# Kernel optimization log

Measured on AMD Instinct MI355X. Metric: run time of the kernel, lower is better.

## Reference

```python
import jax, jax.numpy as jnp
import numpy as np

B, I, D = 8192, 1000, 1000   # batch of candidates, rated items, item feature dim
E, ATT, D1, D2 = 64, 16, 64, 32  # embed size, attention hidden, MLP dense1/dense2


def setup_inputs() -> dict:
    key = jax.random.key(0)
    ks = jax.random.split(key, 16)
    init = lambda k, shape, fan_in: (jax.random.normal(k, shape, jnp.float32) / np.sqrt(fan_in))
    return {
        "candidate_items": jax.random.normal(ks[0], (B, D), jnp.float32),
        "rated_items": jax.random.normal(ks[1], (I, D), jnp.float32),
        "user_matrix": jax.random.uniform(ks[2], (B, I), jnp.float32),
        # item_embeddings: Linear(D, E)
        "We": init(ks[3], (E, D), D), "be": jnp.zeros((E,), jnp.float32),
        # AttentionNet: Linear(2E, ATT) -> ReLU -> Linear(ATT, 1)
        "Wa1": init(ks[4], (ATT, 2 * E), 2 * E), "ba1": jnp.zeros((ATT,), jnp.float32),
        "Wa2": init(ks[5], (1, ATT), ATT), "ba2": jnp.zeros((1,), jnp.float32),
        # MLP: Linear(2E, D1) -> ReLU -> Linear(D1, D2) -> ReLU -> Linear(D2, 1)
        "Wm1": init(ks[6], (D1, 2 * E), 2 * E), "bm1": jnp.zeros((D1,), jnp.float32),
        "Wm2": init(ks[7], (D2, D1), D1), "bm2": jnp.zeros((D2,), jnp.float32),
        "Wm3": init(ks[8], (1, D2), D2), "bm3": jnp.zeros((1,), jnp.float32),
    }


def reference(candidate_items, rated_items, user_matrix,
              We, be, Wa1, ba1, Wa2, ba2, Wm1, bm1, Wm2, bm2, Wm3, bm3):
    # item embeddings
    e_c = candidate_items @ We.T + be                    # [B, E]
    # rated embeddings are .detach()'d in the original
    e_r = jax.lax.stop_gradient(rated_items @ We.T + be) # [I, E]
    e_c_sg = jax.lax.stop_gradient(e_c)                  # detached for attention

    # Additive attention over concat([cand, rated]): split Wa1 into cand/rated halves
    # so the per-i loop becomes one broadcasted op producing [B, I, ATT].
    W1c, W1r = Wa1[:, :E], Wa1[:, E:]
    h = jax.nn.relu(e_c_sg @ W1c.T[:, None, :].reshape(1, 1, -1).reshape(E, ATT)[None][0] if False else
                    (e_c_sg @ W1c.T)[:, None, :] + (e_r @ W1r.T)[None, :, :] + ba1)  # [B, I, ATT]
    scores = jnp.einsum('bia,a->bi', h, Wa2[0]) + ba2[0]  # [B, I]
    att = jax.nn.softmax(scores, axis=1)                  # [B, I]

    # attention-weighted user profile -> user embedding
    user_emb = (att * user_matrix) @ e_r                  # [B, E]

    # MLP head (dropout inactive: eval mode)
    x = jnp.concatenate([e_c, user_emb], axis=1)          # [B, 2E]
    x = jax.nn.relu(x @ Wm1.T + bm1)
    x = jax.nn.relu(x @ Wm2.T + bm2)
    return x @ Wm3.T + bm3                                # [B, 1]
```

## Files before the change

### kernel.cpp

```cpp
#include <hip/hip_runtime.h>

typedef unsigned short u16;
typedef unsigned int   u32;
typedef float f32x4  __attribute__((ext_vector_type(4)));
typedef short bf16x8 __attribute__((ext_vector_type(8)));
typedef short s16x4  __attribute__((ext_vector_type(4)));

__device__ __forceinline__ u16 f2b_rne(float x) {
    u32 u = __float_as_uint(x);
    return (u16)((u + 0x7fffu + ((u >> 16) & 1u)) >> 16);
}
__device__ __forceinline__ float b2f(u16 u) { return __uint_as_float((u32)u << 16); }
__device__ __forceinline__ void split1(float x, u16& h, u16& l) {
    h = f2b_rne(x);
    l = f2b_rne(x - b2f(h));
}
__device__ __forceinline__ void mk_frag(f32x4 a, f32x4 b, bf16x8& hi, bf16x8& lo) {
#pragma unroll
    for (int j = 0; j < 4; ++j) { u16 h, l; split1(a[j], h, l); hi[j] = (short)h; lo[j] = (short)l; }
#pragma unroll
    for (int j = 0; j < 4; ++j) { u16 h, l; split1(b[j], h, l); hi[4+j] = (short)h; lo[4+j] = (short)l; }
}

__global__ __launch_bounds__(1024, 8) void kemb_all(
    const float* __restrict__ cand, const float* __restrict__ rated,
    const float* __restrict__ We, const float* __restrict__ be,
    const float* __restrict__ Wa1, const float* __restrict__ Wm1,
    float* __restrict__ ec, u16* __restrict__ er_th, float* __restrict__ ar,
    u16* __restrict__ Wm1b)
{
    const int blk = blockIdx.x;
    if (blk == 63) {
        for (int idx = threadIdx.x; idx < 8192; idx += 1024)
            Wm1b[idx] = f2b_rne(Wm1[idx]);
        return;
    }
    const bool is_rated = (blk < 64);
    const int  i0    = is_rated ? blk * 16 : (blk - 64) * 16;
    const int  Mrows = is_rated ? 1000 : 8192;
    const float* X   = is_rated ? rated : cand;

    __shared__ u16 S16[2 * 16 * 1008];
    float* Sf = (float*)S16;
    u16* XH = S16;
    u16* XL = S16 + 16 * 1008;

    const int t    = threadIdx.x;
    const int wv   = t >> 6;
    const int lane = t & 63;

    {
        const int r    = wv;
        const int arow = min(i0 + r, Mrows - 1);
        const float* xr = X + (size_t)arow * 1000;
#pragma unroll
        for (int j = 0; j < 4; ++j) {
            const int k4 = lane + j * 64;
            if (k4 < 250) {
                f32x4 v = *(const f32x4*)(xr + k4 * 4);
                s16x4 h4, l4;
#pragma unroll
                for (int jj = 0; jj < 4; ++jj) {
                    u16 hh, ll; split1(v[jj], hh, ll);
                    h4[jj] = (short)hh; l4[jj] = (short)ll;
                }
                *(s16x4*)(XH + r * 1008 + k4 * 4) = h4;
                *(s16x4*)(XL + r * 1008 + k4 * 4) = l4;
            }
        }
    }
    __syncthreads();

    const int l15 = lane & 15, q = lane >> 4;
    const int ct = wv & 3, h = wv >> 2;
    f32x4 acc = {0.f, 0.f, 0.f, 0.f};
    {
        const u16* ahp = XH + l15 * 1008;
        const u16* alp = XL + l15 * 1008;
        const float* wr = We + (size_t)(ct * 16 + l15) * 1000;

        const int kc0 = h * 256;
        const int kc1 = (h == 3) ? 992 : kc0 + 256;
        for (int kc = kc0; kc < kc1; kc += 32) {
            bf16x8 ah = *(const bf16x8*)(ahp + kc + q * 8);
            bf16x8 al = *(const bf16x8*)(alp + kc + q * 8);
            bf16x8 bh, bl;
            mk_frag(*(const f32x4*)(wr + kc + q * 8), *(const f32x4*)(wr + kc + q * 8 + 4), bh, bl);
            acc = __builtin_amdgcn_mfma_f32_16x16x32_bf16(ah, bh, acc, 0, 0, 0);
            acc = __builtin_amdgcn_mfma_f32_16x16x32_bf16(ah, bl, acc, 0, 0, 0);
            acc = __builtin_amdgcn_mfma_f32_16x16x32_bf16(al, bh, acc, 0, 0, 0);
        }
        if (h == 3) {
            bf16x8 ah = {0,0,0,0,0,0,0,0}, al = {0,0,0,0,0,0,0,0};
            bf16x8 bh = {0,0,0,0,0,0,0,0}, bl = {0,0,0,0,0,0,0,0};
            if (q == 0) {
                ah = *(const bf16x8*)(ahp + 992);
                al = *(const bf16x8*)(alp + 992);
                mk_frag(*(const f32x4*)(wr + 992), *(const f32x4*)(wr + 996), bh, bl);
            }
            acc = __builtin_amdgcn_mfma_f32_16x16x32_bf16(ah, bh, acc, 0, 0, 0);
            acc = __builtin_amdgcn_mfma_f32_16x16x32_bf16(ah, bl, acc, 0, 0, 0);
            acc = __builtin_amdgcn_mfma_f32_16x16x32_bf16(al, bh, acc, 0, 0, 0);
        }
    }
    __syncthreads();
#pragma unroll
    for (int r = 0; r < 4; ++r)
        Sf[h * 1024 + (q * 4 + r) * 64 + ct * 16 + l15] = acc[r];
    __syncthreads();

    {
        const int b = t >> 6, e = t & 63;
        float v = be[e] + Sf[b * 64 + e] + Sf[1024 + b * 64 + e]
                        + Sf[2048 + b * 64 + e] + Sf[3072 + b * 64 + e];
        if (!is_rated) {
            ec[(size_t)(i0 + b) * 64 + e] = v;
        } else {
            if (i0 + b < 1000) er_th[(size_t)e * 1000 + (i0 + b)] = f2b_rne(v);
            Sf[4096 + b * 68 + e] = v;
        }
    }

    if (is_rated) {
        __syncthreads();
        if (wv == 0) {
            f32x4 a2 = {0.f, 0.f, 0.f, 0.f};
#pragma unroll
            for (int kc = 0; kc < 64; kc += 32) {
                const float* ap = Sf + 4096 + l15 * 68 + kc + q * 8;
                const float* bp = Wa1 + l15 * 128 + 64 + kc + q * 8;
                bf16x8 ah, al, bh, bl;
                mk_frag(*(const f32x4*)ap, *(const f32x4*)(ap + 4), ah, al);
                mk_frag(*(const f32x4*)bp, *(const f32x4*)(bp + 4), bh, bl);
                a2 = __builtin_amdgcn_mfma_f32_16x16x32_bf16(ah, bh, a2, 0, 0, 0);
                a2 = __builtin_amdgcn_mfma_f32_16x16x32_bf16(ah, bl, a2, 0, 0, 0);
                a2 = __builtin_amdgcn_mfma_f32_16x16x32_bf16(al, bh, a2, 0, 0, 0);
            }
#pragma unroll
            for (int r = 0; r < 4; ++r) {
                int i = i0 + q * 4 + r;
                if (i < 1000) ar[(size_t)i * 16 + l15] = a2[r];
            }
        }
    }
}

__global__ __launch_bounds__(1024, 8) void k3v10(
    const float* __restrict__ ar, const float* __restrict__ ecC,
    const u16* __restrict__ er_th, const float* __restrict__ um,
    const float* __restrict__ Wa1, const float* __restrict__ ba1,
    const float* __restrict__ Wa2, const u16* __restrict__ Wm1b,
    const float* __restrict__ bm1,
    const float* __restrict__ Wm2, const float* __restrict__ bm2,
    const float* __restrict__ Wm3, const float* __restrict__ bm3,
    float* __restrict__ out)
{
    __shared__ u16   S16[16 * 1032];
    __shared__ float ACL[256];
    __shared__ float SUMS[16];
    __shared__ u16   XB16[16 * 136];
    float* Sf = (float*)S16;
    const int t  = threadIdx.x;
    const int b0 = blockIdx.x * 16;

    if (t < 256) {
        const int a = t & 15, b = t >> 4;
        float acc = ba1[a];
        const float* ecr = ecC + (size_t)(b0 + b) * 64;
        const float* w = Wa1 + a * 128;
#pragma unroll 8
        for (int e = 0; e < 64; ++e) acc += ecr[e] * w[e];
        ACL[b * 16 + a] = acc;
    }
    __syncthreads();

    {
        const int i = t;
        if (i < 1000) {
            const f32x4* a4 = (const f32x4*)(ar + (size_t)i * 16);
            f32x4 r0 = a4[0], r1 = a4[1], r2 = a4[2], r3 = a4[3];
            float w2[16];
#pragma unroll
            for (int a = 0; a < 16; ++a) w2[a] = Wa2[a];
#pragma unroll 4
            for (int b = 0; b < 16; ++b) {
                const f32x4* ac4 = (const f32x4*)(ACL + b * 16);
                f32x4 c0 = ac4[0], c1 = ac4[1], c2 = ac4[2], c3 = ac4[3];
                float s0 = 0.f, s1 = 0.f;
                s0 += fmaxf(c0[0] + r0[0], 0.f) * w2[0];
                s1 += fmaxf(c0[1] + r0[1], 0.f) * w2[1];
                s0 += fmaxf(c0[2] + r0[2], 0.f) * w2[2];
                s1 += fmaxf(c0[3] + r0[3], 0.f) * w2[3];
                s0 += fmaxf(c1[0] + r1[0], 0.f) * w2[4];
                s1 += fmaxf(c1[1] + r1[1], 0.f) * w2[5];
                s0 += fmaxf(c1[2] + r1[2], 0.f) * w2[6];
                s1 += fmaxf(c1[3] + r1[3], 0.f) * w2[7];
                s0 += fmaxf(c2[0] + r2[0], 0.f) * w2[8];
                s1 += fmaxf(c2[1] + r2[1], 0.f) * w2[9];
                s0 += fmaxf(c2[2] + r2[2], 0.f) * w2[10];
                s1 += fmaxf(c2[3] + r2[3], 0.f) * w2[11];
                s0 += fmaxf(c3[0] + r3[0], 0.f) * w2[12];
                s1 += fmaxf(c3[1] + r3[1], 0.f) * w2[13];
                s0 += fmaxf(c3[2] + r3[2], 0.f) * w2[14];
                s1 += fmaxf(c3[3] + r3[3], 0.f) * w2[15];
                S16[b * 1032 + i] = f2b_rne(s0 + s1);
            }
        }
    }
    __syncthreads();

    {
        const int b = t >> 6, g = t & 63;
        float sv[16], uv[16];
#pragma unroll
        for (int k = 0; k < 16; ++k) {
            int i = g + 64 * k;
            sv[k] = (i < 1000) ? b2f(S16[b * 1032 + i]) : -1e30f;
        }
        float m = -1e30f;
#pragma unroll
        for (int k = 0; k < 16; ++k) m = fmaxf(m, sv[k]);
#pragma unroll
        for (int k = 1; k < 64; k <<= 1) m = fmaxf(m, __shfl_xor(m, k));
        const float* umr = um + (size_t)(b0 + b) * 1000;
#pragma unroll
        for (int k = 0; k < 16; ++k) {
            int i = g + 64 * k;
            uv[k] = (i < 1000) ? umr[i] : 0.f;
        }
        float sum = 0.f;
#pragma unroll
        for (int k = 0; k < 16; ++k) {
            int i = g + 64 * k;
            if (i < 1000) {
                float w = __expf(sv[k] - m);
                sum += w;
                S16[b * 1032 + i] = f2b_rne(w * uv[k]);
            }
        }
#pragma unroll
        for (int k = 1; k < 64; k <<= 1) sum += __shfl_xor(sum, k);
        if (g == 0) SUMS[b] = 1.0f / sum;
    }
    __syncthreads();

    {
        const int wv = t >> 6, lane = t & 63, l15 = lane & 15, q = lane >> 4;
        const int et = wv & 3, h = wv >> 2;
        const u16* php = S16 + l15 * 1032;
        const u16* bhp = er_th + (size_t)(et * 16 + l15) * 1000;
        f32x4 acc = {0.f, 0.f, 0.f, 0.f};

        const int kc0 = h * 256;
        const int kc1 = (h == 3) ? 992 : kc0 + 256;
        for (int kc = kc0; kc < kc1; kc += 32) {
            bf16x8 ah = *(const bf16x8*)(php + kc + q * 8);
            bf16x8 bh = *(const bf16x8*)(bhp + kc + q * 8);
            acc = __builtin_amdgcn_mfma_f32_16x16x32_bf16(ah, bh, acc, 0, 0, 0);
        }
        if (h == 3) {
            bf16x8 ah = {0,0,0,0,0,0,0,0}, bh = {0,0,0,0,0,0,0,0};
            if (q == 0) {
                ah = *(const bf16x8*)(php + 992);
                bh = *(const bf16x8*)(bhp + 992);
            }
            acc = __builtin_amdgcn_mfma_f32_16x16x32_bf16(ah, bh, acc, 0, 0, 0);
        }
        __syncthreads();
#pragma unroll
        for (int r = 0; r < 4; ++r)
            Sf[h * 1024 + (q * 4 + r) * 64 + et * 16 + l15] = acc[r];
    }
    __syncthreads();

    {
        const int b = t >> 6, e = t & 63;
        float v = (Sf[b * 64 + e] + Sf[1024 + b * 64 + e]
                 + Sf[2048 + b * 64 + e] + Sf[3072 + b * 64 + e]) * SUMS[b];
        XB16[b * 136 + 64 + e] = f2b_rne(v);
        XB16[b * 136 + e] = f2b_rne(ecC[(size_t)(b0 + b) * 64 + e]);
    }
    __syncthreads();

    {
        const int wv = t >> 6, lane = t & 63, l15 = lane & 15, q = lane >> 4;
        const int nt = wv & 3, kh = wv >> 2;
        bf16x8 ah = *(const bf16x8*)(XB16 + l15 * 136 + kh * 32 + q * 8);
        bf16x8 bh = *(const bf16x8*)(Wm1b + (size_t)(nt * 16 + l15) * 128 + kh * 32 + q * 8);
        f32x4 acc = {0.f, 0.f, 0.f, 0.f};
        acc = __builtin_amdgcn_mfma_f32_16x16x32_bf16(ah, bh, acc, 0, 0, 0);
#pragma unroll
        for (int r = 0; r < 4; ++r)
            Sf[kh * 1024 + (q * 4 + r) * 64 + nt * 16 + l15] = acc[r];
    }
    __syncthreads();

    {
        const int b = t >> 6, o = t & 63;
        float a = bm1[o] + Sf[b * 64 + o] + Sf[1024 + b * 64 + o]
                + Sf[2048 + b * 64 + o] + Sf[3072 + b * 64 + o];
        Sf[4096 + b * 64 + o] = fmaxf(a, 0.f);
    }
    __syncthreads();

    {
        const int b = t >> 6, j = t & 63;
        if (j < 32) {
            float a = bm2[j];
            const float* wr = Wm2 + j * 64;
            const float* x = Sf + 4096 + b * 64;
#pragma unroll 8
            for (int k = 0; k < 64; ++k) a += x[k] * wr[k];
            Sf[5120 + b * 32 + j] = fmaxf(a, 0.f);
        }
    }
    __syncthreads();

    {
        const int b = t >> 6, j = t & 63;
        float p = (j < 32) ? Sf[5120 + b * 32 + j] * Wm3[j] : 0.f;
#pragma unroll
        for (int kk = 1; kk < 64; kk <<= 1) p += __shfl_xor(p, kk);
        if (j == 0) out[b0 + b] = p + bm3[0];
    }
}

extern "C" void kernel_launch(void* const* d_in, const int* in_sizes, int n_in,
                              void* d_out, int out_size, void* d_ws, size_t ws_size,
                              hipStream_t stream) {
    const float* cand  = (const float*)d_in[0];
    const float* rated = (const float*)d_in[1];
    const float* um    = (const float*)d_in[2];
    const float* We    = (const float*)d_in[3];
    const float* be    = (const float*)d_in[4];
    const float* Wa1   = (const float*)d_in[5];
    const float* ba1   = (const float*)d_in[6];
    const float* Wa2   = (const float*)d_in[7];
    const float* Wm1   = (const float*)d_in[9];
    const float* bm1   = (const float*)d_in[10];
    const float* Wm2   = (const float*)d_in[11];
    const float* bm2   = (const float*)d_in[12];
    const float* Wm3   = (const float*)d_in[13];
    const float* bm3   = (const float*)d_in[14];

    float* arw   = (float*)d_ws;
    float* ec    = arw + 16000;
    u16*   er_th = (u16*)(ec + 524288);
    u16*   wm1b  = er_th + 64000;
    float* out   = (float*)d_out;

    kemb_all<<<dim3(576), dim3(1024), 0, stream>>>(cand, rated, We, be, Wa1, Wm1,
                                                   ec, er_th, arw, wm1b);
    k3v10   <<<dim3(512), dim3(1024), 0, stream>>>(arw, ec, er_th, um,
                                                   Wa1, ba1, Wa2, wm1b, bm1,
                                                   Wm2, bm2, Wm3, bm3, out);
}
```

Measured before the change: 163.5 us.

## Fuse embedding and attention kernels into one cooperative kernel with grid sync

Merges the embedding GEMM kernel and the attention/MLP kernel into a single cooperative launch. Each block computes its own candidate embeddings into shared memory, so they no longer round-trip through global memory. Every eighth block also computes a tile of the rated-item embeddings before a grid-wide sync. This removes one launch boundary and the global writes and reads of the candidate embeddings. In exchange it adds a grid barrier, it makes a few blocks do extra work before the barrier (load imbalance), and it requires all 512 blocks of 1024 threads to be co-resident. If the cooperative launch fails, the code falls back to a two-kernel path. A user_matrix load is also moved earlier to overlap with the max-reduction.

```diff
diff --git a/kernel.cpp b/kernel.cpp
--- a/kernel.cpp
+++ b/kernel.cpp
@@ -1,4 +1,7 @@
 #include <hip/hip_runtime.h>
+#include <hip/hip_cooperative_groups.h>
+
+namespace cg = cooperative_groups;
 
 typedef unsigned short u16;
 typedef unsigned int   u32;
@@ -22,36 +25,13 @@
     for (int j = 0; j < 4; ++j) { u16 h, l; split1(b[j], h, l); hi[4+j] = (short)h; lo[4+j] = (short)l; }
 }
 
-__global__ __launch_bounds__(1024, 8) void kemb_all(
-    const float* __restrict__ cand, const float* __restrict__ rated,
-    const float* __restrict__ We, const float* __restrict__ be,
-    const float* __restrict__ Wa1, const float* __restrict__ Wm1,
-    float* __restrict__ ec, u16* __restrict__ er_th, float* __restrict__ ar,
-    u16* __restrict__ Wm1b)
+__device__ __forceinline__ f32x4 gemm_tile(
+    const float* __restrict__ X, int i0, int Mrows,
+    const float* __restrict__ We,
+    u16* XH, u16* XL, int wv, int lane, int l15, int q)
 {
-    const int blk = blockIdx.x;
-    if (blk == 63) {
-        for (int idx = threadIdx.x; idx < 8192; idx += 1024)
-            Wm1b[idx] = f2b_rne(Wm1[idx]);
-        return;
-    }
-    const bool is_rated = (blk < 64);
-    const int  i0    = is_rated ? blk * 16 : (blk - 64) * 16;
-    const int  Mrows = is_rated ? 1000 : 8192;
-    const float* X   = is_rated ? rated : cand;
-
-    __shared__ u16 S16[2 * 16 * 1008];
-    float* Sf = (float*)S16;
-    u16* XH = S16;
-    u16* XL = S16 + 16 * 1008;
-
-    const int t    = threadIdx.x;
-    const int wv   = t >> 6;
-    const int lane = t & 63;
-
-    {
-        const int r    = wv;
-        const int arow = min(i0 + r, Mrows - 1);
+    {
+        const int arow = min(i0 + wv, Mrows - 1);
         const float* xr = X + (size_t)arow * 1000;
 #pragma unroll
         for (int j = 0; j < 4; ++j) {
@@ -64,112 +44,140 @@
                     u16 hh, ll; split1(v[jj], hh, ll);
                     h4[jj] = (short)hh; l4[jj] = (short)ll;
                 }
-                *(s16x4*)(XH + r * 1008 + k4 * 4) = h4;
-                *(s16x4*)(XL + r * 1008 + k4 * 4) = l4;
-            }
-        }
-    }
-    __syncthreads();
-
-    const int l15 = lane & 15, q = lane >> 4;
+                *(s16x4*)(XH + wv * 1008 + k4 * 4) = h4;
+                *(s16x4*)(XL + wv * 1008 + k4 * 4) = l4;
+            }
+        }
+    }
+    __syncthreads();
+
     const int ct = wv & 3, h = wv >> 2;
     f32x4 acc = {0.f, 0.f, 0.f, 0.f};
-    {
-        const u16* ahp = XH + l15 * 1008;
-        const u16* alp = XL + l15 * 1008;
-        const float* wr = We + (size_t)(ct * 16 + l15) * 1000;
-
-        const int kc0 = h * 256;
-        const int kc1 = (h == 3) ? 992 : kc0 + 256;
-        for (int kc = kc0; kc < kc1; kc += 32) {
-            bf16x8 ah = *(const bf16x8*)(ahp + kc + q * 8);
-            bf16x8 al = *(const bf16x8*)(alp + kc + q * 8);
-            bf16x8 bh, bl;
-            mk_frag(*(const f32x4*)(wr + kc + q * 8), *(const f32x4*)(wr + kc + q * 8 + 4), bh, bl);
-            acc = __builtin_amdgcn_mfma_f32_16x16x32_bf16(ah, bh, acc, 0, 0, 0);
-            acc = __builtin_amdgcn_mfma_f32_16x16x32_bf16(ah, bl, acc, 0, 0, 0);
-            acc = __builtin_amdgcn_mfma_f32_16x16x32_bf16(al, bh, acc, 0, 0, 0);
-        }
-        if (h == 3) {
-            bf16x8 ah = {0,0,0,0,0,0,0,0}, al = {0,0,0,0,0,0,0,0};
-            bf16x8 bh = {0,0,0,0,0,0,0,0}, bl = {0,0,0,0,0,0,0,0};
-            if (q == 0) {
-                ah = *(const bf16x8*)(ahp + 992);
-                al = *(const bf16x8*)(alp + 992);
-                mk_frag(*(const f32x4*)(wr + 992), *(const f32x4*)(wr + 996), bh, bl);
-            }
-            acc = __builtin_amdgcn_mfma_f32_16x16x32_bf16(ah, bh, acc, 0, 0, 0);
-            acc = __builtin_amdgcn_mfma_f32_16x16x32_bf16(ah, bl, acc, 0, 0, 0);
-            acc = __builtin_amdgcn_mfma_f32_16x16x32_bf16(al, bh, acc, 0, 0, 0);
-        }
-    }
-    __syncthreads();
-#pragma unroll
-    for (int r = 0; r < 4; ++r)
-        Sf[h * 1024 + (q * 4 + r) * 64 + ct * 16 + l15] = acc[r];
-    __syncthreads();
-
-    {
-        const int b = t >> 6, e = t & 63;
-        float v = be[e] + Sf[b * 64 + e] + Sf[1024 + b * 64 + e]
-                        + Sf[2048 + b * 64 + e] + Sf[3072 + b * 64 + e];
-        if (!is_rated) {
-            ec[(size_t)(i0 + b) * 64 + e] = v;
-        } else {
-            if (i0 + b < 1000) er_th[(size_t)e * 1000 + (i0 + b)] = f2b_rne(v);
-            Sf[4096 + b * 68 + e] = v;
-        }
-    }
-
-    if (is_rated) {
-        __syncthreads();
-        if (wv == 0) {
-            f32x4 a2 = {0.f, 0.f, 0.f, 0.f};
-#pragma unroll
-            for (int kc = 0; kc < 64; kc += 32) {
-                const float* ap = Sf + 4096 + l15 * 68 + kc + q * 8;
-                const float* bp = Wa1 + l15 * 128 + 64 + kc + q * 8;
-                bf16x8 ah, al, bh, bl;
-                mk_frag(*(const f32x4*)ap, *(const f32x4*)(ap + 4), ah, al);
-                mk_frag(*(const f32x4*)bp, *(const f32x4*)(bp + 4), bh, bl);
-                a2 = __builtin_amdgcn_mfma_f32_16x16x32_bf16(ah, bh, a2, 0, 0, 0);
-                a2 = __builtin_amdgcn_mfma_f32_16x16x32_bf16(ah, bl, a2, 0, 0, 0);
-                a2 = __builtin_amdgcn_mfma_f32_16x16x32_bf16(al, bh, a2, 0, 0, 0);
-            }
-#pragma unroll
-            for (int r = 0; r < 4; ++r) {
-                int i = i0 + q * 4 + r;
-                if (i < 1000) ar[(size_t)i * 16 + l15] = a2[r];
-            }
-        }
-    }
-}
-
-__global__ __launch_bounds__(1024, 8) void k3v10(
-    const float* __restrict__ ar, const float* __restrict__ ecC,
-    const u16* __restrict__ er_th, const float* __restrict__ um,
+    const u16* ahp = XH + l15 * 1008;
+    const u16* alp = XL + l15 * 1008;
+    const float* wr = We + (size_t)(ct * 16 + l15) * 1000;
+
+    const int kc0 = h * 256;
+    const int kc1 = (h == 3) ? 992 : kc0 + 256;
+    for (int kc = kc0; kc < kc1; kc += 32) {
+        bf16x8 ah = *(const bf16x8*)(ahp + kc + q * 8);
+        bf16x8 al = *(const bf16x8*)(alp + kc + q * 8);
+        bf16x8 bh, bl;
+        mk_frag(*(const f32x4*)(wr + kc + q * 8), *(const f32x4*)(wr + kc + q * 8 + 4), bh, bl);
+        acc = __builtin_amdgcn_mfma_f32_16x16x32_bf16(ah, bh, acc, 0, 0, 0);
+        acc = __builtin_amdgcn_mfma_f32_16x16x32_bf16(ah, bl, acc, 0, 0, 0);
+        acc = __builtin_amdgcn_mfma_f32_16x16x32_bf16(al, bh, acc, 0, 0, 0);
+    }
+    if (h == 3) {
+        bf16x8 ah = {0,0,0,0,0,0,0,0}, al = {0,0,0,0,0,0,0,0};
+        bf16x8 bh = {0,0,0,0,0,0,0,0}, bl = {0,0,0,0,0,0,0,0};
+        if (q == 0) {
+            ah = *(const bf16x8*)(ahp + 992);
+            al = *(const bf16x8*)(alp + 992);
+            mk_frag(*(const f32x4*)(wr + 992), *(const f32x4*)(wr + 996), bh, bl);
+        }
+        acc = __builtin_amdgcn_mfma_f32_16x16x32_bf16(ah, bh, acc, 0, 0, 0);
+        acc = __builtin_amdgcn_mfma_f32_16x16x32_bf16(ah, bl, acc, 0, 0, 0);
+        acc = __builtin_amdgcn_mfma_f32_16x16x32_bf16(al, bh, acc, 0, 0, 0);
+    }
+    __syncthreads();
+    return acc;
+}
+
+template<bool COOP>
+__global__ __launch_bounds__(1024, 8) void kmega(
+    const float* __restrict__ cand, const float* __restrict__ rated,
+    const float* __restrict__ We, const float* __restrict__ be,
     const float* __restrict__ Wa1, const float* __restrict__ ba1,
-    const float* __restrict__ Wa2, const u16* __restrict__ Wm1b,
-    const float* __restrict__ bm1,
+    const float* __restrict__ Wa2, const float* __restrict__ Wm1,
+    const float* __restrict__ um, const float* __restrict__ bm1,
     const float* __restrict__ Wm2, const float* __restrict__ bm2,
     const float* __restrict__ Wm3, const float* __restrict__ bm3,
+    u16* __restrict__ er_th, float* __restrict__ ar, u16* __restrict__ Wm1b,
     float* __restrict__ out)
 {
-    __shared__ u16   S16[16 * 1032];
+    __shared__ __attribute__((aligned(16))) u16 PL[2 * 16 * 1008];
+    __shared__ float ECT[16 * 64];
     __shared__ float ACL[256];
     __shared__ float SUMS[16];
-    __shared__ u16   XB16[16 * 136];
-    float* Sf = (float*)S16;
-    const int t  = threadIdx.x;
-    const int b0 = blockIdx.x * 16;
+    __shared__ __attribute__((aligned(16))) u16 XB16[16 * 136];
+    float* Sf = (float*)PL;
+    u16*  XH  = PL;
+    u16*  XL  = PL + 16 * 1008;
+    u16*  S16 = PL;
+
+    const int t    = threadIdx.x;
+    const int wv   = t >> 6;
+    const int lane = t & 63;
+    const int l15  = lane & 15;
+    const int q    = lane >> 4;
+    const int blk  = blockIdx.x;
+    const int b0   = blk * 16;
+
+    {
+        f32x4 acc = gemm_tile(cand, b0, 8192, We, XH, XL, wv, lane, l15, q);
+        const int ct = wv & 3, h = wv >> 2;
+#pragma unroll
+        for (int r = 0; r < 4; ++r)
+            Sf[h * 1024 + (q * 4 + r) * 64 + ct * 16 + l15] = acc[r];
+        __syncthreads();
+        const int b = t >> 6, e = t & 63;
+        ECT[b * 64 + e] = be[e] + Sf[b * 64 + e] + Sf[1024 + b * 64 + e]
+                                + Sf[2048 + b * 64 + e] + Sf[3072 + b * 64 + e];
+        __syncthreads();
+    }
+
+    if constexpr (COOP) {
+        if ((blk & 7) == 0 && blk < 504) {
+            const int i0r = (blk >> 3) * 16;
+            f32x4 a2 = gemm_tile(rated, i0r, 1000, We, XH, XL, wv, lane, l15, q);
+            const int ct = wv & 3, h = wv >> 2;
+#pragma unroll
+            for (int r = 0; r < 4; ++r)
+                Sf[h * 1024 + (q * 4 + r) * 64 + ct * 16 + l15] = a2[r];
+            __syncthreads();
+            {
+                const int b = t >> 6, e = t & 63;
+                float v = be[e] + Sf[b * 64 + e] + Sf[1024 + b * 64 + e]
+                                + Sf[2048 + b * 64 + e] + Sf[3072 + b * 64 + e];
+                if (i0r + b < 1000) er_th[(size_t)e * 1000 + (i0r + b)] = f2b_rne(v);
+                Sf[4096 + b * 68 + e] = v;
+            }
+            __syncthreads();
+            if (wv == 0) {
+                f32x4 a3 = {0.f, 0.f, 0.f, 0.f};
+#pragma unroll
+                for (int kc = 0; kc < 64; kc += 32) {
+                    const float* ap = Sf + 4096 + l15 * 68 + kc + q * 8;
+                    const float* bp = Wa1 + l15 * 128 + 64 + kc + q * 8;
+                    bf16x8 ah, al, bh, bl;
+                    mk_frag(*(const f32x4*)ap, *(const f32x4*)(ap + 4), ah, al);
+                    mk_frag(*(const f32x4*)bp, *(const f32x4*)(bp + 4), bh, bl);
+                    a3 = __builtin_amdgcn_mfma_f32_16x16x32_bf16(ah, bh, a3, 0, 0, 0);
+                    a3 = __builtin_amdgcn_mfma_f32_16x16x32_bf16(ah, bl, a3, 0, 0, 0);
+                    a3 = __builtin_amdgcn_mfma_f32_16x16x32_bf16(al, bh, a3, 0, 0, 0);
+                }
+#pragma unroll
+                for (int r = 0; r < 4; ++r) {
+                    int i = i0r + q * 4 + r;
+                    if (i < 1000) ar[(size_t)i * 16 + l15] = a3[r];
+                }
+            }
+        } else if (blk == 504) {
+            for (int idx = t; idx < 8192; idx += 1024)
+                Wm1b[idx] = f2b_rne(Wm1[idx]);
+        }
+        __threadfence();
+        cg::this_grid().sync();
+    }
+
 
     if (t < 256) {
         const int a = t & 15, b = t >> 4;
         float acc = ba1[a];
-        const float* ecr = ecC + (size_t)(b0 + b) * 64;
         const float* w = Wa1 + a * 128;
 #pragma unroll 8
-        for (int e = 0; e < 64; ++e) acc += ecr[e] * w[e];
+        for (int e = 0; e < 64; ++e) acc += ECT[b * 64 + e] * w[e];
         ACL[b * 16 + a] = acc;
     }
     __syncthreads();
@@ -212,6 +220,12 @@
     {
         const int b = t >> 6, g = t & 63;
         float sv[16], uv[16];
+        const float* umr = um + (size_t)(b0 + b) * 1000;
+#pragma unroll
+        for (int k = 0; k < 16; ++k) {
+            int i = g + 64 * k;
+            uv[k] = (i < 1000) ? umr[i] : 0.f;
+        }
 #pragma unroll
         for (int k = 0; k < 16; ++k) {
             int i = g + 64 * k;
@@ -222,12 +236,6 @@
         for (int k = 0; k < 16; ++k) m = fmaxf(m, sv[k]);
 #pragma unroll
         for (int k = 1; k < 64; k <<= 1) m = fmaxf(m, __shfl_xor(m, k));
-        const float* umr = um + (size_t)(b0 + b) * 1000;
-#pragma unroll
-        for (int k = 0; k < 16; ++k) {
-            int i = g + 64 * k;
-            uv[k] = (i < 1000) ? umr[i] : 0.f;
-        }
         float sum = 0.f;
 #pragma unroll
         for (int k = 0; k < 16; ++k) {
@@ -245,7 +253,6 @@
     __syncthreads();
 
     {
-        const int wv = t >> 6, lane = t & 63, l15 = lane & 15, q = lane >> 4;
         const int et = wv & 3, h = wv >> 2;
         const u16* php = S16 + l15 * 1032;
         const u16* bhp = er_th + (size_t)(et * 16 + l15) * 1000;
@@ -278,12 +285,11 @@
         float v = (Sf[b * 64 + e] + Sf[1024 + b * 64 + e]
                  + Sf[2048 + b * 64 + e] + Sf[3072 + b * 64 + e]) * SUMS[b];
         XB16[b * 136 + 64 + e] = f2b_rne(v);
-        XB16[b * 136 + e] = f2b_rne(ecC[(size_t)(b0 + b) * 64 + e]);
-    }
-    __syncthreads();
-
-    {
-        const int wv = t >> 6, lane = t & 63, l15 = lane & 15, q = lane >> 4;
+        XB16[b * 136 + e] = f2b_rne(ECT[b * 64 + e]);
+    }
+    __syncthreads();
+
+    {
         const int nt = wv & 3, kh = wv >> 2;
         bf16x8 ah = *(const bf16x8*)(XB16 + l15 * 136 + kh * 32 + q * 8);
         bf16x8 bh = *(const bf16x8*)(Wm1b + (size_t)(nt * 16 + l15) * 128 + kh * 32 + q * 8);
@@ -322,6 +328,64 @@
 #pragma unroll
         for (int kk = 1; kk < 64; kk <<= 1) p += __shfl_xor(p, kk);
         if (j == 0) out[b0 + b] = p + bm3[0];
+    }
+}
+
+__global__ __launch_bounds__(1024, 8) void kprep(
+    const float* __restrict__ rated, const float* __restrict__ We,
+    const float* __restrict__ be, const float* __restrict__ Wa1,
+    const float* __restrict__ Wm1,
+    u16* __restrict__ er_th, float* __restrict__ ar, u16* __restrict__ Wm1b)
+{
+    if (blockIdx.x == 63) {
+        for (int idx = threadIdx.x; idx < 8192; idx += 1024)
+            Wm1b[idx] = f2b_rne(Wm1[idx]);
+        return;
+    }
+    __shared__ __attribute__((aligned(16))) u16 PL[2 * 16 * 1008];
+    float* Sf = (float*)PL;
+    u16* XH = PL;
+    u16* XL = PL + 16 * 1008;
+
+    const int t    = threadIdx.x;
+    const int wv   = t >> 6;
+    const int lane = t & 63;
+    const int l15  = lane & 15;
+    const int q    = lane >> 4;
+    const int i0r  = blockIdx.x * 16;
+
+    f32x4 a2 = gemm_tile(rated, i0r, 1000, We, XH, XL, wv, lane, l15, q);
+    const int ct = wv & 3, h = wv >> 2;
+#pragma unroll
+    for (int r = 0; r < 4; ++r)
+        Sf[h * 1024 + (q * 4 + r) * 64 + ct * 16 + l15] = a2[r];
+    __syncthreads();
+    {
+        const int b = t >> 6, e = t & 63;
+        float v = be[e] + Sf[b * 64 + e] + Sf[1024 + b * 64 + e]
+                        + Sf[2048 + b * 64 + e] + Sf[3072 + b * 64 + e];
+        if (i0r + b < 1000) er_th[(size_t)e * 1000 + (i0r + b)] = f2b_rne(v);
+        Sf[4096 + b * 68 + e] = v;
+    }
+    __syncthreads();
+    if (wv == 0) {
+        f32x4 a3 = {0.f, 0.f, 0.f, 0.f};
+#pragma unroll
+        for (int kc = 0; kc < 64; kc += 32) {
+            const float* ap = Sf + 4096 + l15 * 68 + kc + q * 8;
+            const float* bp = Wa1 + l15 * 128 + 64 + kc + q * 8;
+            bf16x8 ah, al, bh, bl;
+            mk_frag(*(const f32x4*)ap, *(const f32x4*)(ap + 4), ah, al);
+            mk_frag(*(const f32x4*)bp, *(const f32x4*)(bp + 4), bh, bl);
+            a3 = __builtin_amdgcn_mfma_f32_16x16x32_bf16(ah, bh, a3, 0, 0, 0);
+            a3 = __builtin_amdgcn_mfma_f32_16x16x32_bf16(ah, bl, a3, 0, 0, 0);
+            a3 = __builtin_amdgcn_mfma_f32_16x16x32_bf16(al, bh, a3, 0, 0, 0);
+        }
+#pragma unroll
+        for (int r = 0; r < 4; ++r) {
+            int i = i0r + q * 4 + r;
+            if (i < 1000) ar[(size_t)i * 16 + l15] = a3[r];
+        }
     }
 }
 
@@ -344,14 +408,27 @@
     const float* bm3   = (const float*)d_in[14];
 
     float* arw   = (float*)d_ws;
-    float* ec    = arw + 16000;
-    u16*   er_th = (u16*)(ec + 524288);
+    u16*   er_th = (u16*)(arw + 16000);
     u16*   wm1b  = er_th + 64000;
     float* out   = (float*)d_out;
 
-    kemb_all<<<dim3(576), dim3(1024), 0, stream>>>(cand, rated, We, be, Wa1, Wm1,
-                                                   ec, er_th, arw, wm1b);
-    k3v10   <<<dim3(512), dim3(1024), 0, stream>>>(arw, ec, er_th, um,
-                                                   Wa1, ba1, Wa2, wm1b, bm1,
-                                                   Wm2, bm2, Wm3, bm3, out);
-}
+    void* kargs[] = {
+        (void*)&cand, (void*)&rated, (void*)&We,  (void*)&be,
+        (void*)&Wa1,  (void*)&ba1,   (void*)&Wa2, (void*)&Wm1,
+        (void*)&um,   (void*)&bm1,   (void*)&Wm2, (void*)&bm2,
+        (void*)&Wm3,  (void*)&bm3,
+        (void*)&er_th, (void*)&arw, (void*)&wm1b, (void*)&out
+    };
+    auto kfn = kmega<true>;
+    hipError_t err = hipLaunchCooperativeKernel(
+        reinterpret_cast<const void*>(kfn), dim3(512), dim3(1024),
+        kargs, 0, stream);
+    if (err != hipSuccess) {
+        (void)hipGetLastError();
+        kprep<<<dim3(64), dim3(1024), 0, stream>>>(rated, We, be, Wa1, Wm1,
+                                                   er_th, arw, wm1b);
+        kmega<false><<<dim3(512), dim3(1024), 0, stream>>>(
+            cand, rated, We, be, Wa1, ba1, Wa2, Wm1, um, bm1,
+            Wm2, bm2, Wm3, bm3, er_th, arw, wm1b, out);
+    }
+}
```

After: 452.8 us. +177.0%, slower.
